# Kernel tuning notes

Hardware: AMD Instinct MI355X
Metric: run time of the kernel (lower is better)

The kernel has to match this reference:

```python
import jax, jax.numpy as jnp
import numpy as np

B, V = 128, 128000
NEG_INF = float('-inf')


def _apply_top_k(logits, top_ks):
    vocab = logits.shape[-1]
    valid_k = jnp.where(top_ks > 0, jnp.minimum(top_ks, vocab), vocab)  # [B]
    order = jnp.argsort(-logits, axis=-1)                 # descending sort indices [B,V]
    sorted_logits = jnp.take_along_axis(logits, order, axis=-1)
    ranks = jnp.arange(vocab)[None, :]                    # [1,V]
    keep = ranks < valid_k[:, None]
    masked_sorted = jnp.where(keep, sorted_logits, NEG_INF)
    rows = jnp.arange(logits.shape[0])[:, None]
    return jnp.zeros_like(logits).at[rows, order].set(masked_sorted)


def _apply_top_p(logits, top_ps):
    order = jnp.argsort(-logits, axis=-1)
    sorted_logits = jnp.take_along_axis(logits, order, axis=-1)
    sorted_probs = jax.nn.softmax(sorted_logits, axis=-1)
    cum = jnp.cumsum(sorted_probs, axis=-1)
    keep = cum < top_ps[:, None]
    keep = keep.at[:, 0].set(True)                        # always keep the top token
    masked_sorted = jnp.where(keep, sorted_logits, NEG_INF)
    rows = jnp.arange(logits.shape[0])[:, None]
    return jnp.zeros_like(logits).at[rows, order].set(masked_sorted)


def setup_inputs() -> dict:
    key = jax.random.key(0)
    k1, k2, k3, k4, k5 = jax.random.split(key, 5)
    logits = jax.random.normal(k1, (B, V), dtype=jnp.float32) * 4.0
    temperatures = jax.random.uniform(k2, (B,), dtype=jnp.float32) + 0.5  # [0.5, 1.5)
    top_ks = jax.random.randint(k3, (B,), 0, 100, dtype=jnp.int64)        # 0 -> disabled
    top_ps = jax.random.uniform(k4, (B,), dtype=jnp.float32)
    # uniform noise; reference converts to Exp(1) via -log(u)
    exp_noise_u = jax.random.uniform(k5, (B, V), dtype=jnp.float32, minval=1e-12, maxval=1.0)
    return {"logits": logits, "temperatures": temperatures, "top_ks": top_ks,
            "top_ps": top_ps, "exp_noise_u": exp_noise_u}


def reference(logits, temperatures, top_ks, top_ps, exp_noise_u):
    x = logits.astype(jnp.float32) / temperatures[:, None]
    x = _apply_top_k(x, top_ks)
    x = _apply_top_p(x, top_ps)
    probs = jax.nn.softmax(x, axis=-1)
    q = jnp.clip(-jnp.log(exp_noise_u), 1e-10)            # Exp(1) samples, clamped like torch
    sample_tokens = jnp.argmax(probs / q, axis=-1)
    return sample_tokens
```

## Files before the change

kernel.cpp:

```cpp
#include <hip/hip_runtime.h>
#include <math.h>

#define SA 8
#define SEGE 8
#define SEGM 8
#define NB 4096
#define TAA 512
#define HS 256
#define TBB 1024
#define SCT 256
#define CH (NB / SCT)
#define CAPSEG 512
#define GTOT (SA * CAPSEG)
#define MAXM1 16
#define GB1 16384
#define SUBC 512
#define EQC 64
#define FXS 1099511627776.0f
#define FXI (1.0f / 1099511627776.0f)

typedef unsigned u32;
typedef unsigned long long u64;

struct ScanSh {
  u32 axc[SCT]; float axe[SCT];
  u32 sufc[SCT]; float sufe[SCT];
  int cbin[SCT]; u32 cca[SCT]; float cea[SCT];
  int fbin[SCT]; u32 fca[SCT]; float fea[SCT];
};

__device__ __forceinline__ u32 f2key(float f) {
  u32 u = __float_as_uint(f);
  return u ^ ((u >> 31) ? 0xFFFFFFFFu : 0x80000000u);
}
__device__ __forceinline__ int is_mode0(int k, int V) {
  return (k >= 1 && k <= 256 && k < V);
}

__device__ __forceinline__ float row_max(const float* maxpart, int row) {
  float mm = maxpart[row * SA];
  for (int j = 1; j < SA; ++j) mm = fmaxf(mm, maxpart[row * SA + j]);
  return mm;
}

__device__ int find_m1row(const int* topks, int B, int V, int slot, int tid,
                          int* flg, int* outrow) {
  for (int r = tid; r < B; r += blockDim.x) flg[r] = !is_mode0(topks[r], V);
  __syncthreads();
  if (tid == 0) {
    int c = 0, rsel = -1;
    for (int r = 0; r < B; ++r)
      if (flg[r]) { if (c == slot) rsel = r; ++c; }
    *outrow = rsel;
  }
  __syncthreads();
  return *outrow;
}

__device__ void scan_level(const u32* cnt, const u64* e0, ScanSh* ax,
                           u32* sprefix, int* scnt_above, float* sexp_above,
                           float target, int tid) {
  if (tid < SCT) {
    u32 cc = 0; float ce = 0.f; const int base = tid * CH;
    for (int j = 0; j < CH; ++j) { cc += cnt[base + j]; ce += (float)e0[base + j] * FXI; }
    ax->axc[tid] = cc; ax->axe[tid] = ce;
  }
  __syncthreads();
  if (tid == 0) {
    u32 rc = 0; float re = 0.f;
    for (int c = SCT - 1; c >= 0; --c) {
      ax->sufc[c] = rc; ax->sufe[c] = re;
      rc += ax->axc[c]; re += ax->axe[c];
    }
  }
  __syncthreads();
  if (tid < SCT) {
    const int base = tid * CH;
    u32 rc = ax->sufc[tid]; float re = ax->sufe[tid];
    int best = -1; u32 bca = 0; float bea = 0.f;
    int fb = -1; u32 ffca = 0; float ffea = 0.f;
    for (int b = base + CH - 1; b >= base; --b) {
      u32 c = cnt[b]; float ebv = (float)e0[b] * FXI;
      bool cross = (c > 0) && ((re + ebv) >= target);
      if (cross && best < 0) { best = b; bca = rc; bea = re; }
      if (c > 0) { fb = b; ffca = rc; ffea = re; }
      rc += c; re += ebv;
    }
    ax->cbin[tid] = best; ax->cca[tid] = bca; ax->cea[tid] = bea;
    ax->fbin[tid] = fb; ax->fca[tid] = ffca; ax->fea[tid] = ffea;
  }
  __syncthreads();
  if (tid == 0) {
    int bsel = -1; u32 ca = 0; float ea = 0.f;
    for (int c = 0; c < SCT; ++c) {
      int b = ax->cbin[c];
      if (b > bsel) { bsel = b; ca = ax->cca[c]; ea = ax->cea[c]; }
    }
    if (bsel < 0) {
      for (int c = 0; c < SCT; ++c) {
        int b = ax->fbin[c];
        if (b >= 0 && (bsel < 0 || b < bsel)) { bsel = b; ca = ax->fca[c]; ea = ax->fea[c]; }
      }
    }
    if (bsel < 0) bsel = 0;
    *sprefix = (u32)bsel;
    *scnt_above = (int)ca;
    *sexp_above = ea;
  }
  __syncthreads();
}

__global__ __launch_bounds__(TAA) void kA(const float* __restrict__ logits,
                                          const float* __restrict__ temps,
                                          const int* __restrict__ topks,
                                          float* __restrict__ maxpart,
                                          u32* __restrict__ scnt,
                                          float* __restrict__ candv,
                                          int* __restrict__ candi,
                                          u32* __restrict__ zp, size_t zwords,
                                          int V) {
  const int row = blockIdx.x, seg = blockIdx.y, tid = threadIdx.x;
  __shared__ u32 cnt[NB];
  __shared__ float sm[TAA];
  __shared__ u32 cs[HS];
  __shared__ int bb[HS];
  __shared__ int lcnt;
  __shared__ u32 sT;
  {
    const size_t gid = ((size_t)blockIdx.y * gridDim.x + blockIdx.x) * TAA + tid;
    const size_t stride = (size_t)gridDim.x * gridDim.y * TAA;
    for (size_t i = gid; i < zwords; i += stride) zp[i] = 0;
  }
  const int k = topks[row];
  const int m0 = is_mode0(k, V);
  const float t = temps[row];
  const float* lr = logits + (size_t)row * V;
  const float4* l4 = (const float4*)lr;
  const int n4 = V >> 2;
  const int q0 = (int)((long long)seg * n4 / SA);
  const int q1 = (int)((long long)(seg + 1) * n4 / SA);
  float rmx = -INFINITY;
  if (m0) {
    for (int i = tid; i < NB; i += TAA) cnt[i] = 0;
    if (tid == 0) lcnt = 0;
    __syncthreads();
    for (int i = q0 + tid; i < q1; i += TAA) {
      float4 v = l4[i];
      rmx = fmaxf(rmx, fmaxf(fmaxf(v.x, v.y), fmaxf(v.z, v.w)));
      atomicAdd(&cnt[f2key(v.x) >> 20], 1u);
      atomicAdd(&cnt[f2key(v.y) >> 20], 1u);
      atomicAdd(&cnt[f2key(v.z) >> 20], 1u);
      atomicAdd(&cnt[f2key(v.w) >> 20], 1u);
    }
    if (seg == SA - 1)
      for (int i = (n4 << 2) + tid; i < V; i += TAA) {
        float x = lr[i];
        rmx = fmaxf(rmx, x);
        atomicAdd(&cnt[f2key(x) >> 20], 1u);
      }
  } else {
    for (int i = q0 + tid; i < q1; i += TAA) {
      float4 v = l4[i];
      rmx = fmaxf(rmx, fmaxf(fmaxf(v.x, v.y), fmaxf(v.z, v.w)));
    }
    if (seg == SA - 1)
      for (int i = (n4 << 2) + tid; i < V; i += TAA) rmx = fmaxf(rmx, lr[i]);
  }
  sm[tid] = rmx;
  __syncthreads();
  for (int s = TAA >> 1; s > 0; s >>= 1) {
    if (tid < s) sm[tid] = fmaxf(sm[tid], sm[tid + s]);
    __syncthreads();
  }
  if (tid == 0) maxpart[row * SA + seg] = sm[0] / t;
  if (!m0) return;
  if (tid < HS) {
    u32 cc = 0; const int base = tid * (NB / HS);
    for (int j = 0; j < NB / HS; ++j) cc += cnt[base + j];
    cs[tid] = cc;
  }
  __syncthreads();
  if (tid == 0) {
    u32 rc = 0;
    for (int c = HS - 1; c >= 0; --c) { u32 tmp = cs[c]; cs[c] = rc; rc += tmp; }
  }
  __syncthreads();
  const int kk = (k > 256) ? 256 : k;
  if (tid < HS) {
    const int base = tid * (NB / HS);
    u32 rc = cs[tid]; int best = -1;
    for (int b = base + NB / HS - 1; b >= base; --b) {
      u32 c = cnt[b];
      if (c && best < 0 && (int)(rc + c) >= kk) best = b;
      rc += c;
    }
    bb[tid] = best;
  }
  __syncthreads();
  if (tid == 0) {
    int bsel = -1;
    for (int c = 0; c < HS; ++c) if (bb[c] > bsel) bsel = bb[c];
    if (bsel < 0) { for (int b = 0; b < NB; ++b) if (cnt[b]) { bsel = b; break; } }
    if (bsel < 0) bsel = 0;
    sT = ((u32)bsel) << 20;
  }
  __syncthreads();
  const u32 T = sT;
  const size_t cbase = ((size_t)row * SA + seg) * CAPSEG;
  for (int i = q0 + tid; i < q1; i += TAA) {
    float4 v = l4[i];
    float vs[4] = {v.x, v.y, v.z, v.w};
#pragma unroll
    for (int j = 0; j < 4; ++j) {
      if (f2key(vs[j]) >= T) {
        int s = atomicAdd(&lcnt, 1);
        if (s < CAPSEG) { candv[cbase + s] = vs[j] / t; candi[cbase + s] = i * 4 + j; }
      }
    }
  }
  if (seg == SA - 1)
    for (int i = (n4 << 2) + tid; i < V; i += TAA) {
      float x = lr[i];
      if (f2key(x) >= T) {
        int s = atomicAdd(&lcnt, 1);
        if (s < CAPSEG) { candv[cbase + s] = x / t; candi[cbase + s] = i; }
      }
    }
  __syncthreads();
  if (tid == 0) { int n = lcnt; if (n > CAPSEG) n = CAPSEG; scnt[row * SA + seg] = (u32)n; }
}

__global__ __launch_bounds__(TBB) void kEH(const float* __restrict__ logits,
                                           const float* __restrict__ temps,
                                           const int* __restrict__ topks,
                                           const float* __restrict__ topps,
                                           const float* __restrict__ noise,
                                           const float* __restrict__ maxpart,
                                           const u32* __restrict__ scnt,
                                           const float* __restrict__ candv,
                                           const int* __restrict__ candi,
                                           float* __restrict__ Sparts,
                                           u32* __restrict__ m1c0,
                                           u64* __restrict__ m1e0,
                                           int* __restrict__ out, int B, int V) {
  const int bx = blockIdx.x, tid = threadIdx.x;
  __shared__ float gv[GTOT]; __shared__ int gi[GTOT];
  __shared__ float sv[CAPSEG]; __shared__ int si[CAPSEG];
  __shared__ float fv[CAPSEG]; __shared__ int fi[CAPSEG];
  __shared__ float pe[CAPSEG];
  __shared__ float rr[TBB]; __shared__ int ri[TBB];
  __shared__ int offs[SA + 1];
  __shared__ u32 dh[256]; __shared__ u32 dsufx[256];
  __shared__ u32 sPrefix; __shared__ int sRemain, sNf, sDig;
  __shared__ int sJ; __shared__ float sZ2;
  __shared__ u32 c0[NB];
  __shared__ u64 e0[NB];
  __shared__ float ss[TBB];
  __shared__ int flg[1024]; __shared__ int srow;

  if (bx >= B) {
    const int e = bx - B;
    const int slot = e / SEGE, seg = e % SEGE;
    if (slot >= MAXM1) return;
    const int row = find_m1row(topks, B, V, slot, tid, flg, &srow);
    if (row < 0) return;
    for (int i = tid; i < NB; i += TBB) { c0[i] = 0; e0[i] = 0ull; }
    __syncthreads();
    const float t = temps[row];
    const float m = row_max(maxpart, row);
    const float* lr = logits + (size_t)row * V;
    const float4* l4 = (const float4*)lr;
    const int n4 = V >> 2;
    const int q0 = (int)((long long)seg * n4 / SEGE);
    const int q1 = (int)((long long)(seg + 1) * n4 / SEGE);
    float ls = 0.f;
    for (int i = q0 + tid; i < q1; i += TBB) {
      float4 v = l4[i];
      float xs[4] = {v.x / t, v.y / t, v.z / t, v.w / t};
#pragma unroll
      for (int j = 0; j < 4; ++j) {
        float ev = expf(xs[j] - m);
        ls += ev;
        u32 b = f2key(xs[j]) >> 20;
        atomicAdd(&c0[b], 1u);
        u64 fx = (u64)(ev * FXS);
        if (fx) atomicAdd(&e0[b], fx);
      }
    }
    if (seg == SEGE - 1)
      for (int i = (n4 << 2) + tid; i < V; i += TBB) {
        float x = lr[i] / t;
        float ev = expf(x - m);
        ls += ev;
        u32 b = f2key(x) >> 20;
        atomicAdd(&c0[b], 1u);
        u64 fx = (u64)(ev * FXS);
        if (fx) atomicAdd(&e0[b], fx);
      }
    ss[tid] = ls;
    __syncthreads();
    for (int s = TBB >> 1; s > 0; s >>= 1) {
      if (tid < s) ss[tid] += ss[tid + s];
      __syncthreads();
    }
    if (tid == 0) Sparts[slot * SEGE + seg] = ss[0];
    for (int b = tid; b < NB; b += TBB) {
      u32 c = c0[b]; if (c) atomicAdd(&m1c0[(size_t)slot * NB + b], c);
      u64 ev = e0[b]; if (ev) atomicAdd(&m1e0[(size_t)slot * NB + b], ev);
    }
    return;
  }

  const int row = bx;
  const int kR = topks[row];
  if (!is_mode0(kR, V)) return;
  if (tid == 0) {
    int o = 0;
    for (int s = 0; s < SA; ++s) {
      offs[s] = o;
      int c = (int)scnt[row * SA + s];
      if (c > CAPSEG) c = CAPSEG;
      if (c < 0) c = 0;
      o += c;
    }
    offs[SA] = o;
  }
  __syncthreads();
  const int g = offs[SA];
  for (int s = 0; s < SA; ++s) {
    const int o = offs[s], c = offs[s + 1] - o;
    const size_t cbase = ((size_t)row * SA + s) * CAPSEG;
    for (int i = tid; i < c; i += TBB) { gv[o + i] = candv[cbase + i]; gi[o + i] = candi[cbase + i]; }
  }
  __syncthreads();
  int kk = kR; if (kk > 256) kk = 256; if (kk > g) kk = g;
  if (tid == 0) { sPrefix = 0u; sRemain = (kk < 1) ? 1 : kk; }
  __syncthreads();
  for (int pass = 0; pass < 4; ++pass) {
    const int shift = 24 - 8 * pass;
    if (tid < 256) dh[tid] = 0;
    if (tid == 0) sDig = -1;
    __syncthreads();
    const u32 pref = sPrefix;
    for (int i = tid; i < g; i += TBB) {
      u32 key = f2key(gv[i]);
      if (pass == 0 || (key >> (shift + 8)) == pref)
        atomicAdd(&dh[(key >> shift) & 0xFFu], 1u);
    }
    __syncthreads();
    if (tid < 256) dsufx[tid] = dh[tid];
    __syncthreads();
    for (int stp = 1; stp < 256; stp <<= 1) {
      u32 addv = 0;
      if (tid < 256 && tid + stp < 256) addv = dsufx[tid + stp];
      __syncthreads();
      if (tid < 256) dsufx[tid] += addv;
      __syncthreads();
    }
    if (tid < 256) {
      u32 excl = dsufx[tid] - dh[tid];
      u32 rem = (u32)sRemain;
      if (dh[tid] && excl < rem && excl + dh[tid] >= rem) sDig = tid;
    }
    __syncthreads();
    if (tid == 0) {
      int d = sDig; if (d < 0) d = 0;
      u32 excl = dsufx[d] - dh[d];
      sRemain -= (int)excl;
      sPrefix = (sPrefix << 8) | (u32)d;
      if (pass == 3) sNf = 0;
    }
    __syncthreads();
  }
  const u32 Tk = sPrefix;
  for (int i = tid; i < g; i += TBB) {
    if (f2key(gv[i]) >= Tk) {
      int s = atomicAdd(&sNf, 1);
      if (s < CAPSEG) { fv[s] = gv[i]; fi[s] = gi[i]; }
    }
  }
  __syncthreads();
  int nf = sNf; if (nf > CAPSEG) nf = CAPSEG;
  for (int i = tid; i < nf; i += TBB) {
    float v = fv[i]; int ix = fi[i];
    int rank = 0;
    for (int j = 0; j < nf; ++j) {
      float vj = fv[j]; int ij = fi[j];
      if (vj > v || (vj == v && ij < ix)) rank++;
    }
    sv[rank] = v; si[rank] = ix;
  }
  __syncthreads();
  const float m = row_max(maxpart, row);
  const float p = topps[row];
  int keff = kR; if (keff > nf) keff = nf;
  for (int j = tid; j < keff; j += TBB) pe[j] = expf(sv[j] - m);
  __syncthreads();
  if (tid == 0) {
    int J = 1; float Z2 = 1.f;
    if (nf > 0 && keff > 0) {
      float Zk = 0.f;
      for (int j = 0; j < keff; ++j) Zk += pe[j];
      float c = 0.f; int Jc = 0;
      for (int j = 0; j < keff; ++j) {
        float pr = pe[j] / Zk;
        c += pr;
        if (c < p) Jc++;
      }
      if (Jc < 1) Jc = 1;
      J = Jc;
      Z2 = 0.f;
      for (int j = 0; j < J && j < keff; ++j) Z2 += pe[j];
    }
    sJ = J; sZ2 = Z2;
  }
  __syncthreads();
  const int J = sJ; const float Z2 = sZ2;
  float best = -1.f; int bidx = 0x7FFFFFFF;
  for (int j = tid; j < J && j < nf; j += TBB) {
    int ix = si[j];
    float u = noise[(size_t)row * V + ix];
    float q = fmaxf(-logf(u), 1e-10f);
    float pr = pe[j] / Z2;
    float rt = pr / q;
    if (rt > best || (rt == best && ix < bidx)) { best = rt; bidx = ix; }
  }
  rr[tid] = best; ri[tid] = bidx;
  __syncthreads();
  for (int s = TBB >> 1; s > 0; s >>= 1) {
    if (tid < s) {
      float ov = rr[tid + s]; int oi = ri[tid + s];
      if (ov > rr[tid] || (ov == rr[tid] && oi < ri[tid])) { rr[tid] = ov; ri[tid] = oi; }
    }
    __syncthreads();
  }
  if (tid == 0) out[row] = (nf > 0) ? ri[0] : 0;
}

__global__ __launch_bounds__(TBB) void kM1(const float* __restrict__ logits,
                                           const float* __restrict__ temps,
                                           const int* __restrict__ topks,
                                           const float* __restrict__ topps,
                                           const float* __restrict__ noise,
                                           const float* __restrict__ maxpart,
                                           const float* __restrict__ Sparts,
                                           const u32* __restrict__ m1c0,
                                           const u64* __restrict__ m1e0,
                                           u64* __restrict__ g1p,
                                           u32* __restrict__ gcnt,
                                           u64* __restrict__ rpack,
                                           u32* __restrict__ rdone,
                                           int* __restrict__ out, int B, int V) {
  const int slot = blockIdx.x, seg = blockIdx.y, tid = threadIdx.x;
  __shared__ int flg[1024]; __shared__ int srow;
  const int row = find_m1row(topks, B, V, slot, tid, flg, &srow);
  if (row < 0) return;

  __shared__ u32 cnt[NB];
  __shared__ u64 e0[NB];
  __shared__ ScanSh ax;
  __shared__ u32 spfx; __shared__ int sca; __shared__ float sea;
  __shared__ float rr[TBB]; __shared__ int ri[TBB];
  for (int i = tid; i < NB; i += TBB) {
    cnt[i] = m1c0[(size_t)slot * NB + i];
    e0[i] = m1e0[(size_t)slot * NB + i];
  }
  __syncthreads();
  float S = 0.f;
  for (int j = 0; j < SEGE; ++j) S += Sparts[slot * SEGE + j];
  const float target = topps[row] * S;
  scan_level(cnt, e0, &ax, &spfx, &sca, &sea, target, tid);
  const u32 pfx = spfx;

  const float t = temps[row];
  const float m = row_max(maxpart, row);
  const float* lr = logits + (size_t)row * V;
  const float* ur = noise + (size_t)row * V;
  const float4* l4 = (const float4*)lr;
  const float4* u4 = (const float4*)ur;
  const int n4 = V >> 2;
  const int q0 = (int)((long long)seg * n4 / SEGM);
  const int q1 = (int)((long long)(seg + 1) * n4 / SEGM);
  const size_t gbase = (size_t)slot * GB1;

  float best = -1.f; int bidx = 0x7FFFFFFF;
  for (int i = q0 + tid; i < q1; i += TBB) {
    float4 xv = l4[i];
    float4 uv = u4[i];
    float xs[4] = {xv.x / t, xv.y / t, xv.z / t, xv.w / t};
    float us[4] = {uv.x, uv.y, uv.z, uv.w};
#pragma unroll
    for (int j = 0; j < 4; ++j) {
      u32 key = f2key(xs[j]);
      u32 bin = key >> 20;
      int idx = i * 4 + j;
      if (bin == pfx) {
        u32 s2 = atomicAdd(&gcnt[slot], 1u);
        if (s2 < GB1)
          atomicExch(&g1p[gbase + s2],
                     ((u64)__float_as_uint(xs[j]) << 32) | (u64)(u32)idx);
      } else if (bin > pfx) {
        float q = fmaxf(-logf(us[j]), 1e-10f);
        float rt = expf(xs[j] - m) / q;
        if (rt > best || (rt == best && idx < bidx)) { best = rt; bidx = idx; }
      }
    }
  }
  if (seg == SEGM - 1)
    for (int i = (n4 << 2) + tid; i < V; i += TBB) {
      float x = lr[i] / t;
      u32 key = f2key(x);
      u32 bin = key >> 20;
      if (bin == pfx) {
        u32 s2 = atomicAdd(&gcnt[slot], 1u);
        if (s2 < GB1)
          atomicExch(&g1p[gbase + s2],
                     ((u64)__float_as_uint(x) << 32) | (u64)(u32)i);
      } else if (bin > pfx) {
        float q = fmaxf(-logf(ur[i]), 1e-10f);
        float rt = expf(x - m) / q;
        if (rt > best || (rt == best && i < bidx)) { best = rt; bidx = i; }
      }
    }
  rr[tid] = best; ri[tid] = bidx;
  __syncthreads();
  for (int s = TBB >> 1; s > 0; s >>= 1) {
    if (tid < s) {
      float ov = rr[tid + s]; int oi = ri[tid + s];
      if (ov > rr[tid] || (ov == rr[tid] && oi < ri[tid])) { rr[tid] = ov; ri[tid] = oi; }
    }
    __syncthreads();
  }
  __shared__ int slast;
  if (tid == 0) {
    if (rr[0] >= 0.f) {
      u64 pk = ((u64)f2key(rr[0]) << 32) | (u64)(0xFFFFFFFFu - (u32)ri[0]);
      atomicMax(&rpack[row], pk);
    }
    __threadfence();
    u32 arr = atomicAdd(&rdone[row], 1u);
    slast = (arr == (u32)(SEGM - 1)) ? 1 : 0;
  }
  __syncthreads();
  if (!slast) return;
  __threadfence();

  __shared__ u32 cnt1[1024]; __shared__ u64 fx1[1024];
  __shared__ u32 csuf[1024]; __shared__ u64 esuf[1024];
  __shared__ float subv[SUBC]; __shared__ int subi[SUBC];
  __shared__ float ssv[SUBC]; __shared__ int ssi[SUBC];
  __shared__ int eqs[EQC];
  __shared__ int scross, sfb, sca1, sns, seqn;
  __shared__ float sea1; __shared__ u32 svstar;

  int nf = (int)atomicAdd(&gcnt[slot], 0u);
  if (nf > GB1) nf = GB1;
  cnt1[tid] = 0; fx1[tid] = 0ull;
  if (tid == 0) { sns = 0; scross = -1; sfb = 0x7FFFFFFF; }
  __syncthreads();
  for (int i = tid; i < nf; i += TBB) {
    u64 p = atomicAdd(&g1p[gbase + i], 0ull);
    float x = __uint_as_float((u32)(p >> 32));
    u32 b = (f2key(x) >> 10) & 0x3FFu;
    float e = expf(x - m);
    atomicAdd(&cnt1[b], 1u);
    u64 fx = (u64)(e * FXS);
    if (fx) atomicAdd(&fx1[b], fx);
  }
  __syncthreads();
  csuf[tid] = cnt1[tid]; esuf[tid] = fx1[tid];
  __syncthreads();
  for (int stp = 1; stp < 1024; stp <<= 1) {
    u32 ca_ = 0; u64 ea_ = 0ull;
    if (tid + stp < 1024) { ca_ = csuf[tid + stp]; ea_ = esuf[tid + stp]; }
    __syncthreads();
    csuf[tid] += ca_; esuf[tid] += ea_;
    __syncthreads();
  }
  {
    u32 c = cnt1[tid];
    if (c) {
      float racc = (float)(esuf[tid] - fx1[tid]) * FXI;
      float ebv = (float)fx1[tid] * FXI;
      if (sea + (racc + ebv) >= target) atomicMax(&scross, tid);
      atomicMin(&sfb, tid);
    }
  }
  __syncthreads();
  if (tid == 0) {
    int cb = scross;
    if (cb < 0) cb = (sfb != 0x7FFFFFFF) ? sfb : 0;
    u32 cAbove = csuf[cb] - cnt1[cb];
    float eAbove = (float)(esuf[cb] - fx1[cb]) * FXI;
    scross = cb;
    sea1 = sea + eAbove;
    sca1 = sca + (int)cAbove;
  }
  __syncthreads();
  const u32 cb = (u32)scross;
  for (int i = tid; i < nf; i += TBB) {
    u64 p = atomicAdd(&g1p[gbase + i], 0ull);
    float x = __uint_as_float((u32)(p >> 32));
    if (((f2key(x) >> 10) & 0x3FFu) == cb) {
      int s2 = atomicAdd(&sns, 1);
      if (s2 < SUBC) { subv[s2] = x; subi[s2] = (int)(u32)(p & 0xFFFFFFFFull); }
    }
  }
  __syncthreads();
  int ns = sns; if (ns > SUBC) ns = SUBC;
  for (int i = tid; i < ns; i += TBB) {
    float v = subv[i]; int ix = subi[i];
    int rank = 0;
    for (int j2 = 0; j2 < ns; ++j2) {
      float vj = subv[j2]; int ij = subi[j2];
      if (vj > v || (vj == v && ij < ix)) rank++;
    }
    ssv[rank] = v; ssi[rank] = ix;
  }
  __syncthreads();
  if (tid == 0) {
    const float p = topps[row];
    float run_n = sea1 / S;
    const int have_above = (sca1 > 0);
    u32 lastkey = 0u; int lastr = 0, laststart = -1, anykept = 0;
    u32 vsel = 0u; int rsel = -1, bstart = 0;
    int j = 0;
    while (j < ns) {
      u32 key = f2key(ssv[j]);
      int c = 1;
      while (j + c < ns && f2key(ssv[j + c]) == key) ++c;
      float e = expf(ssv[j] - m);
      float en = e / S;
      int kept = 0;
      for (int q = 0; q < c; ++q) {
        float nn = run_n + en;
        if (nn < p) { run_n = nn; kept++; } else break;
      }
      if (kept == c) { lastkey = key; lastr = c; laststart = j; anykept = 1; j += c; continue; }
      if (kept > 0) { vsel = key; rsel = kept; bstart = j; }
      else if (anykept) { vsel = lastkey; rsel = lastr; bstart = laststart; }
      else if (have_above) { vsel = key; rsel = 0; bstart = j; }
      else { vsel = key; rsel = 1; bstart = j; }
      break;
    }
    if (rsel < 0) {
      if (anykept) { vsel = lastkey; rsel = lastr; bstart = laststart; }
      else if (ns > 0) {
        vsel = f2key(ssv[0]); bstart = 0;
        rsel = have_above ? 0 : 1;
      } else { vsel = 0u; rsel = 0; bstart = 0; }
    }
    int eqn = rsel;
    if (eqn > EQC) eqn = EQC;
    if (eqn < 0) eqn = 0;
    if (bstart + eqn > ns) eqn = ns - bstart;
    if (eqn < 0) eqn = 0;
    for (int q2 = 0; q2 < eqn; ++q2) eqs[q2] = ssi[bstart + q2];
    seqn = eqn; svstar = vsel;
  }
  __syncthreads();

  const u32 vk = svstar;
  const int eqn = seqn;
  best = -1.f; bidx = 0x7FFFFFFF;
  for (int i = tid; i < nf; i += TBB) {
    u64 p = atomicAdd(&g1p[gbase + i], 0ull);
    float x = __uint_as_float((u32)(p >> 32));
    int ix = (int)(u32)(p & 0xFFFFFFFFull);
    u32 key = f2key(x);
    bool kept = key > vk;
    if (!kept && key == vk) {
      for (int e = 0; e < eqn; ++e) if (eqs[e] == ix) { kept = true; break; }
    }
    if (kept) {
      float q = fmaxf(-logf(ur[ix]), 1e-10f);
      float rt = expf(x - m) / q;
      if (rt > best || (rt == best && ix < bidx)) { best = rt; bidx = ix; }
    }
  }
  rr[tid] = best; ri[tid] = bidx;
  __syncthreads();
  for (int s = TBB >> 1; s > 0; s >>= 1) {
    if (tid < s) {
      float ov = rr[tid + s]; int oi = ri[tid + s];
      if (ov > rr[tid] || (ov == rr[tid] && oi < ri[tid])) { rr[tid] = ov; ri[tid] = oi; }
    }
    __syncthreads();
  }
  if (tid == 0) {
    u64 myPk = 0ull;
    if (rr[0] >= 0.f)
      myPk = ((u64)f2key(rr[0]) << 32) | (u64)(0xFFFFFFFFu - (u32)ri[0]);
    u64 prev = atomicMax(&rpack[row], myPk);
    u64 fin = prev > myPk ? prev : myPk;
    out[row] = (int)(0xFFFFFFFFu - (u32)(fin & 0xFFFFFFFFull));
  }
}

extern "C" void kernel_launch(void* const* d_in, const int* in_sizes, int n_in,
                              void* d_out, int out_size, void* d_ws, size_t ws_size,
                              hipStream_t stream) {
  const float* logits = (const float*)d_in[0];
  const float* temps = (const float*)d_in[1];
  const int* topks = (const int*)d_in[2];
  const float* topps = (const float*)d_in[3];
  const float* noise = (const float*)d_in[4];
  int* out = (int*)d_out;
  const int B = in_sizes[1];
  const int V = in_sizes[0] / B;
  (void)n_in; (void)out_size; (void)ws_size;

  u32* w = (u32*)d_ws;
  size_t o = 0;
  float* maxpart = (float*)(w + o); o += (size_t)B * SA;
  u32* scnt = w + o; o += (size_t)B * SA;
  float* candv = (float*)(w + o); o += (size_t)B * SA * CAPSEG;
  int* candi = (int*)(w + o); o += (size_t)B * SA * CAPSEG;
  if (o & 1) o += 1;
  const size_t zbase = o;
  u64* m1e0 = (u64*)(w + o); o += 2 * (size_t)MAXM1 * NB;
  u32* m1c0 = w + o; o += (size_t)MAXM1 * NB;
  u64* rpack = (u64*)(w + o); o += 2 * (size_t)B;
  u32* rdone = w + o; o += (size_t)B;
  u32* gcnt = w + o; o += MAXM1;
  if (o & 1) o += 1;
  const size_t zwords = o - zbase;
  float* Sparts = (float*)(w + o); o += (size_t)MAXM1 * SEGE;
  if (o & 1) o += 1;
  u64* g1p = (u64*)(w + o); o += 2 * (size_t)MAXM1 * GB1;

  kA<<<dim3(B, SA), TAA, 0, stream>>>(logits, temps, topks, maxpart, scnt,
                                      candv, candi, w + zbase, zwords, V);
  kEH<<<B + MAXM1 * SEGE, TBB, 0, stream>>>(logits, temps, topks, topps, noise,
                                            maxpart, scnt, candv, candi,
                                            Sparts, m1c0, m1e0, out, B, V);
  kM1<<<dim3(MAXM1, SEGM), TBB, 0, stream>>>(logits, temps, topks, topps, noise,
                                             maxpart, Sparts, m1c0, m1e0, g1p,
                                             gcnt, rpack, rdone, out, B, V);
}
```

Before: 223.9 us.

## Move top-p histogram scan and per-bin sample maxima into kEH

The mode-1 (no top-k) histogram blocks now also load the noise and record, per histogram bin, the packed max of exp(x-m)/q with its index in shared memory, then merge it into a global per-slot table. The last-arriving segment block runs the top-p threshold scan and stores the prefix, counts and sums in an aux struct. kM1 no longer rescans the histogram or reads noise for every element. It only collects the boundary-bin candidates and takes the max over bins above the prefix from the precomputed table. This shifts noise reads and log work into the pass that already reads the logits, and adds 64-bit shared atomicMax traffic in the histogram loop.

```diff
diff --git a/kernel.cpp b/kernel.cpp
--- a/kernel.cpp
+++ b/kernel.cpp
@@ -29,6 +29,14 @@
   int fbin[SCT]; u32 fca[SCT]; float fea[SCT];
 };
 
+struct Aux1 {
+  u32 pfx;
+  int ca;
+  float ea;
+  float S;
+  float target;
+};
+
 __device__ __forceinline__ u32 f2key(float f) {
   u32 u = __float_as_uint(f);
   return u ^ ((u >> 31) ? 0xFFFFFFFFu : 0x80000000u);
@@ -45,11 +53,11 @@
 
 __device__ int find_m1row(const int* topks, int B, int V, int slot, int tid,
                           int* flg, int* outrow) {
-  for (int r = tid; r < B; r += blockDim.x) flg[r] = !is_mode0(topks[r], V);
+  for (int r = tid; r < B && r < 1024; r += blockDim.x) flg[r] = !is_mode0(topks[r], V);
   __syncthreads();
   if (tid == 0) {
     int c = 0, rsel = -1;
-    for (int r = 0; r < B; ++r)
+    for (int r = 0; r < B && r < 1024; ++r)
       if (flg[r]) { if (c == slot) rsel = r; ++c; }
     *outrow = rsel;
   }
@@ -242,6 +250,9 @@
                                            float* __restrict__ Sparts,
                                            u32* __restrict__ m1c0,
                                            u64* __restrict__ m1e0,
+                                           u64* __restrict__ m1w,
+                                           u32* __restrict__ rdoneE,
+                                           Aux1* __restrict__ aux,
                                            int* __restrict__ out, int B, int V) {
   const int bx = blockIdx.x, tid = threadIdx.x;
   __shared__ float gv[GTOT]; __shared__ int gi[GTOT];
@@ -255,8 +266,12 @@
   __shared__ int sJ; __shared__ float sZ2;
   __shared__ u32 c0[NB];
   __shared__ u64 e0[NB];
+  __shared__ u64 wtab[NB];
   __shared__ float ss[TBB];
+  __shared__ ScanSh ax;
   __shared__ int flg[1024]; __shared__ int srow;
+  __shared__ u32 spfx; __shared__ int sca; __shared__ float sea;
+  __shared__ float sS; __shared__ int slast;
 
   if (bx >= B) {
     const int e = bx - B;
@@ -264,19 +279,23 @@
     if (slot >= MAXM1) return;
     const int row = find_m1row(topks, B, V, slot, tid, flg, &srow);
     if (row < 0) return;
-    for (int i = tid; i < NB; i += TBB) { c0[i] = 0; e0[i] = 0ull; }
+    for (int i = tid; i < NB; i += TBB) { c0[i] = 0; e0[i] = 0ull; wtab[i] = 0ull; }
     __syncthreads();
     const float t = temps[row];
     const float m = row_max(maxpart, row);
     const float* lr = logits + (size_t)row * V;
+    const float* ur = noise + (size_t)row * V;
     const float4* l4 = (const float4*)lr;
+    const float4* u4 = (const float4*)ur;
     const int n4 = V >> 2;
     const int q0 = (int)((long long)seg * n4 / SEGE);
     const int q1 = (int)((long long)(seg + 1) * n4 / SEGE);
     float ls = 0.f;
     for (int i = q0 + tid; i < q1; i += TBB) {
       float4 v = l4[i];
+      float4 uv = u4[i];
       float xs[4] = {v.x / t, v.y / t, v.z / t, v.w / t};
+      float us[4] = {uv.x, uv.y, uv.z, uv.w};
 #pragma unroll
       for (int j = 0; j < 4; ++j) {
         float ev = expf(xs[j] - m);
@@ -285,6 +304,10 @@
         atomicAdd(&c0[b], 1u);
         u64 fx = (u64)(ev * FXS);
         if (fx) atomicAdd(&e0[b], fx);
+        float q = fmaxf(-logf(us[j]), 1e-10f);
+        float rt = ev / q;
+        u64 wp = ((u64)f2key(rt) << 32) | (u64)(0xFFFFFFFFu - (u32)(i * 4 + j));
+        atomicMax(&wtab[b], wp);
       }
     }
     if (seg == SEGE - 1)
@@ -296,6 +319,10 @@
         atomicAdd(&c0[b], 1u);
         u64 fx = (u64)(ev * FXS);
         if (fx) atomicAdd(&e0[b], fx);
+        float q = fmaxf(-logf(ur[i]), 1e-10f);
+        float rt = ev / q;
+        u64 wp = ((u64)f2key(rt) << 32) | (u64)(0xFFFFFFFFu - (u32)i);
+        atomicMax(&wtab[b], wp);
       }
     ss[tid] = ls;
     __syncthreads();
@@ -303,10 +330,39 @@
       if (tid < s) ss[tid] += ss[tid + s];
       __syncthreads();
     }
-    if (tid == 0) Sparts[slot * SEGE + seg] = ss[0];
+    if (tid == 0)
+      atomicExch((u32*)&Sparts[slot * SEGE + seg], __float_as_uint(ss[0]));
     for (int b = tid; b < NB; b += TBB) {
       u32 c = c0[b]; if (c) atomicAdd(&m1c0[(size_t)slot * NB + b], c);
       u64 ev = e0[b]; if (ev) atomicAdd(&m1e0[(size_t)slot * NB + b], ev);
+      u64 wv = wtab[b]; if (wv) atomicMax(&m1w[(size_t)slot * NB + b], wv);
+    }
+    __syncthreads();
+    if (tid == 0) {
+      __threadfence();
+      u32 arr = atomicAdd(&rdoneE[slot], 1u);
+      slast = (arr == (u32)(SEGE - 1)) ? 1 : 0;
+    }
+    __syncthreads();
+    if (!slast) return;
+    __threadfence();
+
+    for (int i = tid; i < NB; i += TBB) {
+      c0[i] = atomicAdd(&m1c0[(size_t)slot * NB + i], 0u);
+      e0[i] = atomicAdd(&m1e0[(size_t)slot * NB + i], 0ull);
+    }
+    if (tid == 0) {
+      float S = 0.f;
+      for (int j = 0; j < SEGE; ++j)
+        S += __uint_as_float(atomicAdd((u32*)&Sparts[slot * SEGE + j], 0u));
+      sS = S;
+    }
+    __syncthreads();
+    const float target = topps[row] * sS;
+    scan_level(c0, e0, &ax, &spfx, &sca, &sea, target, tid);
+    if (tid == 0) {
+      Aux1 a; a.pfx = spfx; a.ca = sca; a.ea = sea; a.S = sS; a.target = target;
+      aux[slot] = a;
     }
     return;
   }
@@ -443,102 +499,57 @@
                                            const float* __restrict__ topps,
                                            const float* __restrict__ noise,
                                            const float* __restrict__ maxpart,
-                                           const float* __restrict__ Sparts,
-                                           const u32* __restrict__ m1c0,
-                                           const u64* __restrict__ m1e0,
+                                           const Aux1* __restrict__ aux,
+                                           const u64* __restrict__ m1w,
                                            u64* __restrict__ g1p,
                                            u32* __restrict__ gcnt,
-                                           u64* __restrict__ rpack,
-                                           u32* __restrict__ rdone,
+                                           u32* __restrict__ rdoneM,
                                            int* __restrict__ out, int B, int V) {
   const int slot = blockIdx.x, seg = blockIdx.y, tid = threadIdx.x;
   __shared__ int flg[1024]; __shared__ int srow;
   const int row = find_m1row(topks, B, V, slot, tid, flg, &srow);
   if (row < 0) return;
 
-  __shared__ u32 cnt[NB];
-  __shared__ u64 e0[NB];
-  __shared__ ScanSh ax;
-  __shared__ u32 spfx; __shared__ int sca; __shared__ float sea;
-  __shared__ float rr[TBB]; __shared__ int ri[TBB];
-  for (int i = tid; i < NB; i += TBB) {
-    cnt[i] = m1c0[(size_t)slot * NB + i];
-    e0[i] = m1e0[(size_t)slot * NB + i];
-  }
-  __syncthreads();
-  float S = 0.f;
-  for (int j = 0; j < SEGE; ++j) S += Sparts[slot * SEGE + j];
-  const float target = topps[row] * S;
-  scan_level(cnt, e0, &ax, &spfx, &sca, &sea, target, tid);
-  const u32 pfx = spfx;
-
+  const Aux1 a = aux[slot];
+  const u32 pfx = a.pfx;
   const float t = temps[row];
   const float m = row_max(maxpart, row);
   const float* lr = logits + (size_t)row * V;
   const float* ur = noise + (size_t)row * V;
   const float4* l4 = (const float4*)lr;
-  const float4* u4 = (const float4*)ur;
   const int n4 = V >> 2;
   const int q0 = (int)((long long)seg * n4 / SEGM);
   const int q1 = (int)((long long)(seg + 1) * n4 / SEGM);
   const size_t gbase = (size_t)slot * GB1;
 
-  float best = -1.f; int bidx = 0x7FFFFFFF;
   for (int i = q0 + tid; i < q1; i += TBB) {
-    float4 xv = l4[i];
-    float4 uv = u4[i];
-    float xs[4] = {xv.x / t, xv.y / t, xv.z / t, xv.w / t};
-    float us[4] = {uv.x, uv.y, uv.z, uv.w};
+    float4 v = l4[i];
+    float xs[4] = {v.x / t, v.y / t, v.z / t, v.w / t};
 #pragma unroll
     for (int j = 0; j < 4; ++j) {
-      u32 key = f2key(xs[j]);
-      u32 bin = key >> 20;
-      int idx = i * 4 + j;
-      if (bin == pfx) {
+      if ((f2key(xs[j]) >> 20) == pfx) {
         u32 s2 = atomicAdd(&gcnt[slot], 1u);
         if (s2 < GB1)
           atomicExch(&g1p[gbase + s2],
-                     ((u64)__float_as_uint(xs[j]) << 32) | (u64)(u32)idx);
-      } else if (bin > pfx) {
-        float q = fmaxf(-logf(us[j]), 1e-10f);
-        float rt = expf(xs[j] - m) / q;
-        if (rt > best || (rt == best && idx < bidx)) { best = rt; bidx = idx; }
+                     ((u64)__float_as_uint(xs[j]) << 32) | (u64)(u32)(i * 4 + j));
       }
     }
   }
   if (seg == SEGM - 1)
     for (int i = (n4 << 2) + tid; i < V; i += TBB) {
       float x = lr[i] / t;
-      u32 key = f2key(x);
-      u32 bin = key >> 20;
-      if (bin == pfx) {
+      if ((f2key(x) >> 20) == pfx) {
         u32 s2 = atomicAdd(&gcnt[slot], 1u);
         if (s2 < GB1)
           atomicExch(&g1p[gbase + s2],
                      ((u64)__float_as_uint(x) << 32) | (u64)(u32)i);
-      } else if (bin > pfx) {
-        float q = fmaxf(-logf(ur[i]), 1e-10f);
-        float rt = expf(x - m) / q;
-        if (rt > best || (rt == best && i < bidx)) { best = rt; bidx = i; }
-      }
-    }
-  rr[tid] = best; ri[tid] = bidx;
-  __syncthreads();
-  for (int s = TBB >> 1; s > 0; s >>= 1) {
-    if (tid < s) {
-      float ov = rr[tid + s]; int oi = ri[tid + s];
-      if (ov > rr[tid] || (ov == rr[tid] && oi < ri[tid])) { rr[tid] = ov; ri[tid] = oi; }
-    }
-    __syncthreads();
-  }
+      }
+    }
+  __syncthreads();
   __shared__ int slast;
   if (tid == 0) {
-    if (rr[0] >= 0.f) {
-      u64 pk = ((u64)f2key(rr[0]) << 32) | (u64)(0xFFFFFFFFu - (u32)ri[0]);
-      atomicMax(&rpack[row], pk);
-    }
     __threadfence();
-    u32 arr = atomicAdd(&rdone[row], 1u);
+    u32 arr = atomicAdd(&rdoneM[slot], 1u);
     slast = (arr == (u32)(SEGM - 1)) ? 1 : 0;
   }
   __syncthreads();
@@ -549,6 +560,7 @@
   __shared__ u32 csuf[1024]; __shared__ u64 esuf[1024];
   __shared__ float subv[SUBC]; __shared__ int subi[SUBC];
   __shared__ float ssv[SUBC]; __shared__ int ssi[SUBC];
+  __shared__ u64 rrp[TBB];
   __shared__ int eqs[EQC];
   __shared__ int scross, sfb, sca1, sns, seqn;
   __shared__ float sea1; __shared__ u32 svstar;
@@ -582,7 +594,7 @@
     if (c) {
       float racc = (float)(esuf[tid] - fx1[tid]) * FXI;
       float ebv = (float)fx1[tid] * FXI;
-      if (sea + (racc + ebv) >= target) atomicMax(&scross, tid);
+      if (a.ea + (racc + ebv) >= a.target) atomicMax(&scross, tid);
       atomicMin(&sfb, tid);
     }
   }
@@ -593,8 +605,8 @@
     u32 cAbove = csuf[cb] - cnt1[cb];
     float eAbove = (float)(esuf[cb] - fx1[cb]) * FXI;
     scross = cb;
-    sea1 = sea + eAbove;
-    sca1 = sca + (int)cAbove;
+    sea1 = a.ea + eAbove;
+    sca1 = a.ca + (int)cAbove;
   }
   __syncthreads();
   const u32 cb = (u32)scross;
@@ -620,7 +632,7 @@
   __syncthreads();
   if (tid == 0) {
     const float p = topps[row];
-    float run_n = sea1 / S;
+    float run_n = sea1 / a.S;
     const int have_above = (sca1 > 0);
     u32 lastkey = 0u; int lastr = 0, laststart = -1, anykept = 0;
     u32 vsel = 0u; int rsel = -1, bstart = 0;
@@ -630,7 +642,7 @@
       int c = 1;
       while (j + c < ns && f2key(ssv[j + c]) == key) ++c;
       float e = expf(ssv[j] - m);
-      float en = e / S;
+      float en = e / a.S;
       int kept = 0;
       for (int q = 0; q < c; ++q) {
         float nn = run_n + en;
@@ -660,9 +672,13 @@
   }
   __syncthreads();
 
+  u64 best = 0ull;
+  for (int b = (int)pfx + 1 + tid; b < NB; b += TBB) {
+    u64 w = m1w[(size_t)slot * NB + b];
+    if (w > best) best = w;
+  }
   const u32 vk = svstar;
   const int eqn = seqn;
-  best = -1.f; bidx = 0x7FFFFFFF;
   for (int i = tid; i < nf; i += TBB) {
     u64 p = atomicAdd(&g1p[gbase + i], 0ull);
     float x = __uint_as_float((u32)(p >> 32));
@@ -675,26 +691,18 @@
     if (kept) {
       float q = fmaxf(-logf(ur[ix]), 1e-10f);
       float rt = expf(x - m) / q;
-      if (rt > best || (rt == best && ix < bidx)) { best = rt; bidx = ix; }
-    }
-  }
-  rr[tid] = best; ri[tid] = bidx;
+      u64 wp = ((u64)f2key(rt) << 32) | (u64)(0xFFFFFFFFu - (u32)ix);
+      if (wp > best) best = wp;
+    }
+  }
+  rrp[tid] = best;
   __syncthreads();
   for (int s = TBB >> 1; s > 0; s >>= 1) {
-    if (tid < s) {
-      float ov = rr[tid + s]; int oi = ri[tid + s];
-      if (ov > rr[tid] || (ov == rr[tid] && oi < ri[tid])) { rr[tid] = ov; ri[tid] = oi; }
-    }
-    __syncthreads();
-  }
-  if (tid == 0) {
-    u64 myPk = 0ull;
-    if (rr[0] >= 0.f)
-      myPk = ((u64)f2key(rr[0]) << 32) | (u64)(0xFFFFFFFFu - (u32)ri[0]);
-    u64 prev = atomicMax(&rpack[row], myPk);
-    u64 fin = prev > myPk ? prev : myPk;
-    out[row] = (int)(0xFFFFFFFFu - (u32)(fin & 0xFFFFFFFFull));
-  }
+    if (tid < s) { if (rrp[tid + s] > rrp[tid]) rrp[tid] = rrp[tid + s]; }
+    __syncthreads();
+  }
+  if (tid == 0)
+    out[row] = (rrp[0] != 0ull) ? (int)(0xFFFFFFFFu - (u32)(rrp[0] & 0xFFFFFFFFull)) : 0;
 }
 
 extern "C" void kernel_launch(void* const* d_in, const int* in_sizes, int n_in,
@@ -719,22 +727,26 @@
   if (o & 1) o += 1;
   const size_t zbase = o;
   u64* m1e0 = (u64*)(w + o); o += 2 * (size_t)MAXM1 * NB;
+  u64* m1w = (u64*)(w + o); o += 2 * (size_t)MAXM1 * NB;
   u32* m1c0 = w + o; o += (size_t)MAXM1 * NB;
-  u64* rpack = (u64*)(w + o); o += 2 * (size_t)B;
-  u32* rdone = w + o; o += (size_t)B;
   u32* gcnt = w + o; o += MAXM1;
+  u32* rdoneE = w + o; o += MAXM1;
+  u32* rdoneM = w + o; o += MAXM1;
   if (o & 1) o += 1;
   const size_t zwords = o - zbase;
   float* Sparts = (float*)(w + o); o += (size_t)MAXM1 * SEGE;
   if (o & 1) o += 1;
+  Aux1* aux = (Aux1*)(w + o); o += (sizeof(Aux1) / 4) * (size_t)MAXM1 + 4;
+  if (o & 1) o += 1;
   u64* g1p = (u64*)(w + o); o += 2 * (size_t)MAXM1 * GB1;
 
   kA<<<dim3(B, SA), TAA, 0, stream>>>(logits, temps, topks, maxpart, scnt,
                                       candv, candi, w + zbase, zwords, V);
   kEH<<<B + MAXM1 * SEGE, TBB, 0, stream>>>(logits, temps, topks, topps, noise,
                                             maxpart, scnt, candv, candi,
-                                            Sparts, m1c0, m1e0, out, B, V);
+                                            Sparts, m1c0, m1e0, m1w, rdoneE,
+                                            aux, out, B, V);
   kM1<<<dim3(MAXM1, SEGM), TBB, 0, stream>>>(logits, temps, topks, topps, noise,
-                                             maxpart, Sparts, m1c0, m1e0, g1p,
-                                             gcnt, rpack, rdone, out, B, V);
-}
+                                             maxpart, aux, m1w, g1p, gcnt,
+                                             rdoneM, out, B, V);
+}
```

Result: faster. 215.5 us (-3.7%).
